# Kernel tuning notes

Measured on AMD Instinct MI355X. Metric: run time of the kernel, lower is better.

## Reference

```python
import jax, jax.numpy as jnp
import numpy as np

N, D, FIN, FOUT, H = 50000, 16, 256, 128, 128  # nodes, degree, in/out feat, lstm hidden


def setup_inputs() -> dict:
    key = jax.random.key(0)
    ks = jax.random.split(key, 16)
    E = N * D
    s = 1.0 / np.sqrt(H)
    inp = {
        "in_nodes_features": jax.random.normal(ks[0], (N, FIN), jnp.float32),
        "W_proj": jax.random.normal(ks[1], (FOUT, FIN), jnp.float32) * 0.05,
        "a_src": jax.random.normal(ks[2], (FOUT,), jnp.float32) * 0.1,
        "a_trg": jax.random.normal(ks[3], (FOUT,), jnp.float32) * 0.1,
        "W_skip": jax.random.normal(ks[4], (FOUT, FIN), jnp.float32) * 0.05,
        "bias": jnp.zeros((FOUT,), jnp.float32),
        "w_ih_f": jax.random.uniform(ks[5], (4 * H, FOUT), jnp.float32, -s, s),
        "w_hh_f": jax.random.uniform(ks[6], (4 * H, H), jnp.float32, -s, s),
        "b_ih_f": jax.random.uniform(ks[7], (4 * H,), jnp.float32, -s, s),
        "b_hh_f": jax.random.uniform(ks[8], (4 * H,), jnp.float32, -s, s),
        "w_ih_b": jax.random.uniform(ks[9], (4 * H, FOUT), jnp.float32, -s, s),
        "w_hh_b": jax.random.uniform(ks[10], (4 * H, H), jnp.float32, -s, s),
        "b_ih_b": jax.random.uniform(ks[11], (4 * H,), jnp.float32, -s, s),
        "b_hh_b": jax.random.uniform(ks[12], (4 * H,), jnp.float32, -s, s),
    }
    # uniform-degree graph: each node is target of exactly D edges (sorted by target)
    trg = jnp.repeat(jnp.arange(N, dtype=jnp.int32), D)
    src = jax.random.randint(ks[13], (E,), 0, N, dtype=jnp.int32)
    inp["edge_index"] = jnp.stack([src, trg])  # [2, E]
    return inp


def _lstm_final_h(seq, w_ih, w_hh, b_ih, b_hh):
    # seq: [N, T, F] -> final hidden state [N, H]
    h0 = jnp.zeros((seq.shape[0], w_hh.shape[1]), seq.dtype)
    def step(carry, x_t):
        h, c = carry
        gates = x_t @ w_ih.T + h @ w_hh.T + (b_ih + b_hh)
        i, f, g, o = jnp.split(gates, 4, axis=-1)
        c = jax.nn.sigmoid(f) * c + jax.nn.sigmoid(i) * jnp.tanh(g)
        h = jax.nn.sigmoid(o) * jnp.tanh(c)
        return (h, c), None
    (h, _), _ = jax.lax.scan(step, (h0, h0), jnp.swapaxes(seq, 0, 1))
    return h


def reference(in_nodes_features, W_proj, a_src, a_trg, W_skip, bias,
              w_ih_f, w_hh_f, b_ih_f, b_hh_f, w_ih_b, w_hh_b, b_ih_b, b_hh_b,
              edge_index):
    x = in_nodes_features
    n = x.shape[0]
    src, trg = edge_index[0], edge_index[1]
    proj = x @ W_proj.T                                   # [N, FOUT]
    s_src = proj @ a_src                                  # [N]
    s_trg = proj @ a_trg                                  # [N]
    # lift to edges
    scores = jax.nn.leaky_relu(s_src[src] + s_trg[trg], 0.2)   # [E]
    # neighborhood-aware softmax (global max subtraction as in original)
    e = jnp.exp(scores - jnp.max(scores))
    denom = jax.ops.segment_sum(e, trg, num_segments=n)
    att = e / (denom[trg] + 1e-16)                        # [E]
    weighted = proj[src] * att[:, None]                   # [E, FOUT]
    # trg is sorted with uniform degree: reshape to per-node neighbor sequences
    deg = weighted.shape[0] // n
    att_r = att.reshape(n, deg)
    feat_r = weighted.reshape(n, deg, -1)
    order = jnp.argsort(att_r, axis=1)                    # ascending attention, per node
    seq = jnp.take_along_axis(feat_r, order[:, :, None], axis=1)  # [N, D, FOUT]
    # bidirectional LSTM; hn[-1] == backward-direction final hidden
    out = _lstm_final_h(seq[:, ::-1], w_ih_b, w_hh_b, b_ih_b, b_hh_b)  # [N, H]
    # skip + bias + activation (dims differ -> skip_proj)
    out = out + x @ W_skip.T
    out = out + bias
    return jax.nn.leaky_relu(out, 0.01)
```

## Files before the change

### kernel.cpp

```cpp
#include <hip/hip_runtime.h>
#include <hip/hip_bf16.h>
#include <math.h>

#define N_NODES 50000
#define DEG 16
#define FIN 256
#define FOUT 128
#define HID 128
#define FG 512
#define NEDGE (N_NODES*DEG)
#define NCHUNK (N_NODES/16)
#define K5GRID 512

typedef __bf16 bf16x8 __attribute__((ext_vector_type(8)));
typedef float  f32x4  __attribute__((ext_vector_type(4)));

static __device__ __forceinline__ float u2f(unsigned int u){ union {unsigned int u; float f;} v; v.u=u; return v.f; }
static __device__ __forceinline__ unsigned int f2u(float f){ union {float f; unsigned int u;} v; v.f=f; return v.u; }
static __device__ __forceinline__ unsigned short f2bfu(float f){
  unsigned int u = f2u(f);
  unsigned int r = u + 0x7fffu + ((u >> 16) & 1u);
  return (unsigned short)(r >> 16);
}
static __device__ __forceinline__ float bflo(unsigned int u){ return u2f(u << 16); }
static __device__ __forceinline__ float bfhi(unsigned int u){ return u2f(u & 0xffff0000u); }
static __device__ __forceinline__ float rcpf(float x){ return __builtin_amdgcn_rcpf(x); }
static __device__ __forceinline__ float sigm(float x){ return rcpf(1.f + __expf(-x)); }
static __device__ __forceinline__ float tanhx(float x){ return 1.f - 2.f*rcpf(__expf(2.f*x) + 1.f); }

union FU { bf16x8 bf; unsigned short us[8]; uint4 u4; };

__global__ __launch_bounds__(256) void k_w(
    const float* __restrict__ Wp, const float* __restrict__ Ws,
    const float* __restrict__ wih, const float* __restrict__ a_src, const float* __restrict__ a_trg,
    unsigned short* __restrict__ Wch, unsigned short* __restrict__ Wcl,
    unsigned short* __restrict__ wihh, unsigned short* __restrict__ wihl,
    double* __restrict__ vsrc, double* __restrict__ vtrg,
    unsigned int* __restrict__ gmax_key)
{
  const int b = blockIdx.x, tid = threadIdx.x;
  if (b < 256) {
    const float* src = (b < 128) ? (Wp + b*FIN) : (Ws + (b-128)*FIN);
    const float v = src[tid];
    const unsigned short h = f2bfu(v);
    Wch[b*FIN + tid] = h;
    Wcl[b*FIN + tid] = f2bfu(v - u2f((unsigned)h << 16));
  } else if (b < 512) {
    const int row = (b-256)*2 + (tid >> 7);
    const int k   = tid & 127;
    const float v = wih[row*HID + k];
    const unsigned short h = f2bfu(v);
    wihh[row*HID + k] = h;
    wihl[row*HID + k] = f2bfu(v - u2f((unsigned)h << 16));
  } else {
    if (tid == 0) *gmax_key = 0u;
    const int k = tid;
    double s1 = 0.0, s2 = 0.0;
    for (int i = 0; i < FOUT; ++i) {
      const double w = (double)Wp[i*FIN + k];
      s1 += (double)a_src[i] * w;
      s2 += (double)a_trg[i] * w;
    }
    vsrc[k] = s1; vtrg[k] = s2;
  }
}

__global__ __launch_bounds__(256) void k_s(
    const float* __restrict__ x, const double* __restrict__ vsrc, const double* __restrict__ vtrg,
    double* __restrict__ ssrc, double* __restrict__ strg)
{
  const int n = blockIdx.x*256 + threadIdx.x;
  if (n >= N_NODES) return;
  double ss = 0.0, st = 0.0;
  for (int k = 0; k < FIN; k += 4) {
    const float4 xv = *(const float4*)&x[n*FIN + k];
    ss += xv.x*vsrc[k] + xv.y*vsrc[k+1] + xv.z*vsrc[k+2] + xv.w*vsrc[k+3];
    st += xv.x*vtrg[k] + xv.y*vtrg[k+1] + xv.z*vtrg[k+2] + xv.w*vtrg[k+3];
  }
  ssrc[n] = ss; strg[n] = st;
}

template<int KD, int MODE>
__global__ __launch_bounds__(256) void kgemm(
    const float* __restrict__ Af32,
    const unsigned short* __restrict__ Ah_g, const unsigned short* __restrict__ Al_g,
    const unsigned short* __restrict__ Bh_g, const unsigned short* __restrict__ Bl_g,
    const float* __restrict__ bias, float* __restrict__ outf,
    unsigned short* __restrict__ o_h, unsigned short* __restrict__ o_l)
{
  __shared__ unsigned short At[2][128*64];
  __shared__ unsigned short Bt[2][64*64];
  const int tid = threadIdx.x;
  const int bm = blockIdx.x, bn = blockIdx.y;
  const int r0 = bm*128;
  const int wave = tid >> 6, lane = tid & 63, c = lane & 15, q = lane >> 4;
  const int srow = tid >> 3, sg = tid & 7;

  f32x4 acc[2][4];
  #pragma unroll
  for (int rt = 0; rt < 2; ++rt)
    #pragma unroll
    for (int ct = 0; ct < 4; ++ct) acc[rt][ct] = (f32x4){0.f,0.f,0.f,0.f};

  for (int kt = 0; kt < KD/64; ++kt) {
    const int k0 = kt*64;
    __syncthreads();
    #pragma unroll
    for (int rr = 0; rr < 4; ++rr) {
      const int row = rr*32 + srow;
      int grow = r0 + row; if (grow >= N_NODES) grow = N_NODES-1;
      const int ga = grow*KD + k0 + sg*8;
      const int la = row*64 + (((sg ^ (row & 7))) << 3);
      if (MODE == 0) {
        const float4 v0 = *(const float4*)&Af32[ga];
        const float4 v1 = *(const float4*)&Af32[ga + 4];
        union { unsigned short us[8]; uint4 u4; } H, L;
        H.us[0]=f2bfu(v0.x); L.us[0]=f2bfu(v0.x - u2f((unsigned)H.us[0] << 16));
        H.us[1]=f2bfu(v0.y); L.us[1]=f2bfu(v0.y - u2f((unsigned)H.us[1] << 16));
        H.us[2]=f2bfu(v0.z); L.us[2]=f2bfu(v0.z - u2f((unsigned)H.us[2] << 16));
        H.us[3]=f2bfu(v0.w); L.us[3]=f2bfu(v0.w - u2f((unsigned)H.us[3] << 16));
        H.us[4]=f2bfu(v1.x); L.us[4]=f2bfu(v1.x - u2f((unsigned)H.us[4] << 16));
        H.us[5]=f2bfu(v1.y); L.us[5]=f2bfu(v1.y - u2f((unsigned)H.us[5] << 16));
        H.us[6]=f2bfu(v1.z); L.us[6]=f2bfu(v1.z - u2f((unsigned)H.us[6] << 16));
        H.us[7]=f2bfu(v1.w); L.us[7]=f2bfu(v1.w - u2f((unsigned)H.us[7] << 16));
        *(uint4*)&At[0][la] = H.u4;
        *(uint4*)&At[1][la] = L.u4;
      } else {
        *(uint4*)&At[0][la] = *(const uint4*)&Ah_g[ga];
        *(uint4*)&At[1][la] = *(const uint4*)&Al_g[ga];
      }
    }
    #pragma unroll
    for (int rr = 0; rr < 2; ++rr) {
      const int row = rr*32 + srow;
      int wr;
      if (MODE == 0) wr = bn*64 + row;
      else { const int j = bn*64 + row; wr = (j & 3)*HID + (j >> 2); }
      const int ga = wr*KD + k0 + sg*8;
      const int la = row*64 + (((sg ^ (row & 7))) << 3);
      *(uint4*)&Bt[0][la] = *(const uint4*)&Bh_g[ga];
      *(uint4*)&Bt[1][la] = *(const uint4*)&Bl_g[ga];
    }
    __syncthreads();

    #pragma unroll
    for (int s = 0; s < 2; ++s) {
      FU Af[2][2], Bf[4][2];
      #pragma unroll
      for (int rt = 0; rt < 2; ++rt) {
        const int row = wave*32 + rt*16 + c;
        const int ad = row*64 + (((((s<<2)+q) ^ (row & 7))) << 3);
        Af[rt][0].u4 = *(const uint4*)&At[0][ad];
        Af[rt][1].u4 = *(const uint4*)&At[1][ad];
      }
      #pragma unroll
      for (int ct = 0; ct < 4; ++ct) {
        const int row = ct*16 + c;
        const int ad = row*64 + (((((s<<2)+q) ^ (row & 7))) << 3);
        Bf[ct][0].u4 = *(const uint4*)&Bt[0][ad];
        Bf[ct][1].u4 = *(const uint4*)&Bt[1][ad];
      }
      #pragma unroll
      for (int rt = 0; rt < 2; ++rt)
        #pragma unroll
        for (int ct = 0; ct < 4; ++ct) {
          acc[rt][ct] = __builtin_amdgcn_mfma_f32_16x16x32_bf16(Af[rt][0].bf, Bf[ct][0].bf, acc[rt][ct], 0,0,0);
          acc[rt][ct] = __builtin_amdgcn_mfma_f32_16x16x32_bf16(Af[rt][1].bf, Bf[ct][0].bf, acc[rt][ct], 0,0,0);
          acc[rt][ct] = __builtin_amdgcn_mfma_f32_16x16x32_bf16(Af[rt][0].bf, Bf[ct][1].bf, acc[rt][ct], 0,0,0);
        }
    }
  }
  __syncthreads();

  if (MODE == 0 && bn >= 2) {
    #pragma unroll
    for (int ct = 0; ct < 4; ++ct) {
      const int col = bn*64 + ct*16 + c - 128;
      const float bv = bias[col];
      #pragma unroll
      for (int rt = 0; rt < 2; ++rt)
        #pragma unroll
        for (int i = 0; i < 4; ++i) {
          const int row = r0 + wave*32 + rt*16 + q*4 + i;
          if (row < N_NODES) outf[row*FOUT + col] = acc[rt][ct][i] + bv;
        }
    }
  } else {
    #pragma unroll
    for (int rt = 0; rt < 2; ++rt)
      #pragma unroll
      for (int ct = 0; ct < 4; ++ct)
        #pragma unroll
        for (int i = 0; i < 4; ++i) {
          const int lrow = wave*32 + rt*16 + q*4 + i;
          const int lcol = ct*16 + c;
          const float v = acc[rt][ct][i];
          const unsigned short h = f2bfu(v);
          At[0][lrow*64 + lcol] = h;
          if (MODE == 0) At[1][lrow*64 + lcol] = f2bfu(v - u2f((unsigned)h << 16));
        }
    __syncthreads();
    const int ncols = (MODE == 0) ? FOUT : FG;
    #pragma unroll
    for (int rr = 0; rr < 4; ++rr) {
      const int row = rr*32 + srow;
      const int grow = r0 + row;
      if (grow < N_NODES) {
        const int dst = grow*ncols + bn*64 + sg*8;
        *(uint4*)&o_h[dst] = *(const uint4*)&At[0][row*64 + sg*8];
        if (MODE == 0) *(uint4*)&o_l[dst] = *(const uint4*)&At[1][row*64 + sg*8];
      }
    }
  }
}

__global__ __launch_bounds__(256) void k3_scores(
    const double* __restrict__ ssrc, const double* __restrict__ strg,
    const int* __restrict__ esrc, const int* __restrict__ etrg,
    double* __restrict__ scod, unsigned int* __restrict__ gmax_key)
{
  const int n = blockIdx.x*256 + threadIdx.x;
  float lmax = -3.0e38f;
  if (n < N_NODES) {
    const double stn = strg[etrg[n*DEG]];
    #pragma unroll
    for (int j = 0; j < DEG; ++j) {
      const int e = n*DEG + j;
      double sc = ssrc[esrc[e]] + stn;
      sc = (sc > 0.0) ? sc : 0.2*sc;
      scod[e] = sc;
      lmax = fmaxf(lmax, (float)sc);
    }
  }
  #pragma unroll
  for (int off = 32; off > 0; off >>= 1)
    lmax = fmaxf(lmax, __shfl_down(lmax, off, 64));
  __shared__ float wmax[4];
  if ((threadIdx.x & 63) == 0) wmax[threadIdx.x >> 6] = lmax;
  __syncthreads();
  if (threadIdx.x == 0) {
    const float mv = fmaxf(fmaxf(wmax[0], wmax[1]), fmaxf(wmax[2], wmax[3]));
    const unsigned int u = f2u(mv);
    const unsigned int key = (u & 0x80000000u) ? ~u : (u | 0x80000000u);
    atomicMax(gmax_key, key);
  }
}

__global__ __launch_bounds__(256) void k4_att(
    const double* __restrict__ scod, const int* __restrict__ esrc,
    const unsigned int* __restrict__ gmax_key,
    float* __restrict__ atts, int* __restrict__ srcs)
{
  const int n = blockIdx.x*256 + threadIdx.x;
  if (n >= N_NODES) return;
  const unsigned int key = *gmax_key;
  const unsigned int u = (key & 0x80000000u) ? (key ^ 0x80000000u) : ~key;
  const float gmax = u2f(u);

  double sc[DEG]; float av[DEG]; int si[DEG];
  float sum = 0.f;
  #pragma unroll
  for (int j = 0; j < DEG; ++j) {
    sc[j] = scod[n*DEG + j];
    av[j] = __expf((float)sc[j] - gmax);
    sum  += av[j];
    si[j] = esrc[n*DEG + j];
  }
  const float inv = 1.f/(sum + 1e-16f);
  #pragma unroll
  for (int j = 0; j < DEG; ++j) {
    int r = 0;
    #pragma unroll
    for (int k = 0; k < DEG; ++k)
      r += (sc[k] > sc[j]) || (sc[k] == sc[j] && k > j);
    atts[n*DEG + r] = av[j]*inv;
    srcs[n*DEG + r] = si[j];
  }
}

__global__ __launch_bounds__(512, 4) void k5_lstm(
    const __hip_bfloat16* __restrict__ G, const float* __restrict__ whh,
    const float* __restrict__ bih, const float* __restrict__ bhh,
    const float* __restrict__ atts, const int* __restrict__ srcs,
    float* __restrict__ out)
{
  __shared__ unsigned short Bs[32768];
  __shared__ unsigned short hbuf[2][16*128];
  __shared__ float attb[16][16];
  __shared__ int   srcb[16][16];

  const int tid  = threadIdx.x;
  const int wave = tid >> 6;
  const int lane = tid & 63;
  const int c    = lane & 15;
  const int q    = lane >> 4;
  const int fcol = wave*16 + c;
  const int nb0  = q*4;

  #pragma unroll
  for (int j = 0; j < 8; ++j) {
    const int s   = tid + j*512;
    const int sg_ = s >> 11, skt = (s >> 9) & 3, sw8 = (s >> 6) & 7, sl = s & 63;
    const float* p = whh + (((sg_ + 2)*128 + sw8*16 + (sl & 15))*128 + skt*32 + (sl >> 4)*8);
    const float4 v0 = *(const float4*)p;
    const float4 v1 = *(const float4*)(p + 4);
    union { unsigned short us[8]; uint4 u4; } P;
    P.us[0]=f2bfu(v0.x); P.us[1]=f2bfu(v0.y); P.us[2]=f2bfu(v0.z); P.us[3]=f2bfu(v0.w);
    P.us[4]=f2bfu(v1.x); P.us[5]=f2bfu(v1.y); P.us[6]=f2bfu(v1.z); P.us[7]=f2bfu(v1.w);
    *(uint4*)&Bs[s*8] = P.u4;
  }

  FU Brg[2][4];
  #pragma unroll
  for (int g = 0; g < 2; ++g) {
    const float* wr = whh + (g*HID + fcol)*HID + q*8;
    #pragma unroll
    for (int kt = 0; kt < 4; ++kt) {
      const float4 w0 = *(const float4*)(wr + kt*32);
      const float4 w1 = *(const float4*)(wr + kt*32 + 4);
      Brg[g][kt].us[0]=f2bfu(w0.x); Brg[g][kt].us[1]=f2bfu(w0.y);
      Brg[g][kt].us[2]=f2bfu(w0.z); Brg[g][kt].us[3]=f2bfu(w0.w);
      Brg[g][kt].us[4]=f2bfu(w1.x); Brg[g][kt].us[5]=f2bfu(w1.y);
      Brg[g][kt].us[6]=f2bfu(w1.z); Brg[g][kt].us[7]=f2bfu(w1.w);
    }
  }

  float bsum[4];
  #pragma unroll
  for (int g = 0; g < 4; ++g) bsum[g] = bih[g*HID + fcol] + bhh[g*HID + fcol];

  int aoff[4];
  #pragma unroll
  for (int kt = 0; kt < 4; ++kt)
    aoff[kt] = c*128 + (((kt*4 + q) ^ c) & 15)*8;

  const unsigned short* Gu = (const unsigned short*)G;

  for (int chunk = blockIdx.x; chunk < NCHUNK; chunk += K5GRID) {
    const int nb = chunk * 16;
    __syncthreads();
    if (tid < 256) {
      ((float*)attb)[tid] = atts[nb*DEG + tid];
      ((int*)  srcb)[tid] = srcs[nb*DEG + tid];
    }
    __syncthreads();

    float cst[4] = {0.f,0.f,0.f,0.f};
    float hv[4]  = {0.f,0.f,0.f,0.f};
    uint2 pf[4];
    #pragma unroll
    for (int r = 0; r < 4; ++r) {
      const int s = srcb[nb0 + r][0];
      pf[r] = *(const uint2*)(Gu + (size_t)s*FG + fcol*4);
    }

    #pragma unroll 4
    for (int t = 0; t < DEG; ++t) {
      uint2 cur[4]; float at[4];
      #pragma unroll
      for (int r = 0; r < 4; ++r) { cur[r] = pf[r]; at[r] = attb[nb0 + r][t]; }
      if (t < DEG-1) {
        #pragma unroll
        for (int r = 0; r < 4; ++r) {
          const int s = srcb[nb0 + r][t+1];
          pf[r] = *(const uint2*)(Gu + (size_t)s*FG + fcol*4);
        }
      }
      f32x4 acc[4];
      #pragma unroll
      for (int r = 0; r < 4; ++r) {
        acc[0][r] = bsum[0] + at[r]*bflo(cur[r].x);
        acc[1][r] = bsum[1] + at[r]*bfhi(cur[r].x);
        acc[2][r] = bsum[2] + at[r]*bflo(cur[r].y);
        acc[3][r] = bsum[3] + at[r]*bfhi(cur[r].y);
      }
      if (t > 0) {
        __syncthreads();
        const unsigned short* hb = hbuf[(t-1) & 1];
        FU A[4];
        #pragma unroll
        for (int kt = 0; kt < 4; ++kt) A[kt].u4 = *(const uint4*)(hb + aoff[kt]);
        #pragma unroll
        for (int g = 0; g < 2; ++g) {
          #pragma unroll
          for (int kt = 0; kt < 4; ++kt)
            acc[g] = __builtin_amdgcn_mfma_f32_16x16x32_bf16(A[kt].bf, Brg[g][kt].bf, acc[g], 0, 0, 0);
        }
        #pragma unroll
        for (int g = 2; g < 4; ++g) {
          FU Bf[4];
          #pragma unroll
          for (int kt = 0; kt < 4; ++kt)
            Bf[kt].u4 = *(const uint4*)&Bs[((((g-2)*4 + kt)*8 + wave)*64 + lane)*8];
          #pragma unroll
          for (int kt = 0; kt < 4; ++kt)
            acc[g] = __builtin_amdgcn_mfma_f32_16x16x32_bf16(A[kt].bf, Bf[kt].bf, acc[g], 0, 0, 0);
        }
      }
      #pragma unroll
      for (int r = 0; r < 4; ++r) {
        const float ig = sigm (acc[0][r]);
        const float fg = sigm (acc[1][r]);
        const float gg = tanhx(acc[2][r]);
        const float og = sigm (acc[3][r]);
        cst[r] = fg*cst[r] + ig*gg;
        hv[r]  = og*tanhx(cst[r]);
      }
      if (t < DEG-1) {
        unsigned short* hw = hbuf[t & 1];
        #pragma unroll
        for (int r = 0; r < 4; ++r) {
          const float other = __shfl_xor(hv[r], 1, 64);
          if ((c & 1) == 0) {
            const unsigned pack = (unsigned)f2bfu(hv[r]) | ((unsigned)f2bfu(other) << 16);
            const int node = nb0 + r;
            const int k = fcol;
            const int half = node*128 + (((k >> 3) ^ node) & 15)*8 + (k & 7);
            *(unsigned*)(hw + half) = pack;
          }
        }
      }
    }
    #pragma unroll
    for (int r = 0; r < 4; ++r) {
      const int node = nb + nb0 + r;
      const float v = hv[r] + out[node*HID + fcol];
      out[node*HID + fcol] = (v > 0.f) ? v : 0.01f*v;
    }
  }
}

extern "C" void kernel_launch(void* const* d_in, const int* in_sizes, int n_in,
                              void* d_out, int out_size, void* d_ws, size_t ws_size,
                              hipStream_t stream)
{
  (void)in_sizes; (void)n_in; (void)out_size; (void)ws_size;
  const float* x     = (const float*)d_in[0];
  const float* Wp    = (const float*)d_in[1];
  const float* a_src = (const float*)d_in[2];
  const float* a_trg = (const float*)d_in[3];
  const float* Ws    = (const float*)d_in[4];
  const float* bias  = (const float*)d_in[5];
  const float* wih_b = (const float*)d_in[10];
  const float* whh_b = (const float*)d_in[11];
  const float* bih_b = (const float*)d_in[12];
  const float* bhh_b = (const float*)d_in[13];
  const int*   eidx  = (const int*)d_in[14];
  const int* esrc = eidx;
  const int* etrg = eidx + NEDGE;
  float* out = (float*)d_out;

  unsigned char* ws = (unsigned char*)d_ws;
  unsigned int*   gmax = (unsigned int*)(ws + 0);
  unsigned short* Gh   = (unsigned short*)(ws + 256);
  unsigned short* projh= (unsigned short*)(ws + 51200256);
  unsigned short* projl= (unsigned short*)(ws + 64000256);
  double*         scod = (double*)(ws + 51200256);
  float*          atts = (float*) (ws + 64000256);
  int*            srcs = (int*)   (ws + 67200256);
  unsigned short* Wch  = (unsigned short*)(ws + 76800256);
  unsigned short* Wcl  = (unsigned short*)(ws + 76931328);
  unsigned short* wihh = (unsigned short*)(ws + 77062400);
  unsigned short* wihl = (unsigned short*)(ws + 77193472);
  double*         vsrc = (double*)(ws + 77324544);
  double*         vtrg = (double*)(ws + 77326592);
  double*         ssrc = (double*)(ws + 77328640);
  double*         strg = (double*)(ws + 77728640);

  k_w<<<dim3(513), dim3(256), 0, stream>>>(Wp, Ws, wih_b, a_src, a_trg,
                                           Wch, Wcl, wihh, wihl, vsrc, vtrg, gmax);
  k_s<<<dim3((N_NODES+255)/256), dim3(256), 0, stream>>>(x, vsrc, vtrg, ssrc, strg);
  kgemm<FIN,0><<<dim3((N_NODES+127)/128, 4), dim3(256), 0, stream>>>(
      x, (const unsigned short*)0, (const unsigned short*)0, Wch, Wcl, bias, out, projh, projl);
  kgemm<HID,1><<<dim3((N_NODES+127)/128, 8), dim3(256), 0, stream>>>(
      (const float*)0, projh, projl, wihh, wihl, bias, out, Gh, (unsigned short*)0);
  k3_scores<<<dim3((N_NODES+255)/256), dim3(256), 0, stream>>>(ssrc, strg, esrc, etrg, scod, gmax);
  k4_att<<<dim3((N_NODES+255)/256), dim3(256), 0, stream>>>(scod, esrc, gmax, atts, srcs);
  k5_lstm<<<dim3(K5GRID), dim3(512), 0, stream>>>((const __hip_bfloat16*)Gh, whh_b, bih_b, bhh_b, atts, srcs, out);
}
```

Before: 505.6 us.

## Fuse score and attention kernels using per-node max, parallelize score dot products

Merges the edge-score kernel and the softmax/sort kernel into one, replacing the global-max atomic with a per-node max. Per-node max subtraction is mathematically equivalent for the softmax, and it removes a kernel launch, the double-precision score buffer round trip, and the atomic. The node-score kernel now uses one wave per node with a shuffle reduction instead of one thread per node doing a serial 256-element loop, which gives coalesced loads. Source indices are pre-multiplied by the row stride so the LSTM gather skips a multiply. Underflow behaviour can differ slightly from the global-max reference.

```diff
diff --git a/kernel.cpp b/kernel.cpp
--- a/kernel.cpp
+++ b/kernel.cpp
@@ -35,8 +35,7 @@
     const float* __restrict__ wih, const float* __restrict__ a_src, const float* __restrict__ a_trg,
     unsigned short* __restrict__ Wch, unsigned short* __restrict__ Wcl,
     unsigned short* __restrict__ wihh, unsigned short* __restrict__ wihl,
-    double* __restrict__ vsrc, double* __restrict__ vtrg,
-    unsigned int* __restrict__ gmax_key)
+    double* __restrict__ vsrc, double* __restrict__ vtrg)
 {
   const int b = blockIdx.x, tid = threadIdx.x;
   if (b < 256) {
@@ -53,7 +52,6 @@
     wihh[row*HID + k] = h;
     wihl[row*HID + k] = f2bfu(v - u2f((unsigned)h << 16));
   } else {
-    if (tid == 0) *gmax_key = 0u;
     const int k = tid;
     double s1 = 0.0, s2 = 0.0;
     for (int i = 0; i < FOUT; ++i) {
@@ -69,15 +67,19 @@
     const float* __restrict__ x, const double* __restrict__ vsrc, const double* __restrict__ vtrg,
     double* __restrict__ ssrc, double* __restrict__ strg)
 {
-  const int n = blockIdx.x*256 + threadIdx.x;
+  const int wave = threadIdx.x >> 6, lane = threadIdx.x & 63;
+  const int n = blockIdx.x*4 + wave;
   if (n >= N_NODES) return;
-  double ss = 0.0, st = 0.0;
-  for (int k = 0; k < FIN; k += 4) {
-    const float4 xv = *(const float4*)&x[n*FIN + k];
-    ss += xv.x*vsrc[k] + xv.y*vsrc[k+1] + xv.z*vsrc[k+2] + xv.w*vsrc[k+3];
-    st += xv.x*vtrg[k] + xv.y*vtrg[k+1] + xv.z*vtrg[k+2] + xv.w*vtrg[k+3];
-  }
-  ssrc[n] = ss; strg[n] = st;
+  const float4 xv = *(const float4*)&x[n*FIN + lane*4];
+  const double x0 = xv.x, x1 = xv.y, x2 = xv.z, x3 = xv.w;
+  double a = x0*vsrc[lane*4] + x1*vsrc[lane*4+1] + x2*vsrc[lane*4+2] + x3*vsrc[lane*4+3];
+  double b = x0*vtrg[lane*4] + x1*vtrg[lane*4+1] + x2*vtrg[lane*4+2] + x3*vtrg[lane*4+3];
+  #pragma unroll
+  for (int off = 32; off > 0; off >>= 1) {
+    a += __shfl_down(a, off, 64);
+    b += __shfl_down(b, off, 64);
+  }
+  if (lane == 0) { ssrc[n] = a; strg[n] = b; }
 }
 
 template<int KD, int MODE>
@@ -214,57 +216,31 @@
   }
 }
 
-__global__ __launch_bounds__(256) void k3_scores(
+__global__ __launch_bounds__(256) void k34(
     const double* __restrict__ ssrc, const double* __restrict__ strg,
     const int* __restrict__ esrc, const int* __restrict__ etrg,
-    double* __restrict__ scod, unsigned int* __restrict__ gmax_key)
-{
-  const int n = blockIdx.x*256 + threadIdx.x;
-  float lmax = -3.0e38f;
-  if (n < N_NODES) {
-    const double stn = strg[etrg[n*DEG]];
-    #pragma unroll
-    for (int j = 0; j < DEG; ++j) {
-      const int e = n*DEG + j;
-      double sc = ssrc[esrc[e]] + stn;
-      sc = (sc > 0.0) ? sc : 0.2*sc;
-      scod[e] = sc;
-      lmax = fmaxf(lmax, (float)sc);
-    }
-  }
-  #pragma unroll
-  for (int off = 32; off > 0; off >>= 1)
-    lmax = fmaxf(lmax, __shfl_down(lmax, off, 64));
-  __shared__ float wmax[4];
-  if ((threadIdx.x & 63) == 0) wmax[threadIdx.x >> 6] = lmax;
-  __syncthreads();
-  if (threadIdx.x == 0) {
-    const float mv = fmaxf(fmaxf(wmax[0], wmax[1]), fmaxf(wmax[2], wmax[3]));
-    const unsigned int u = f2u(mv);
-    const unsigned int key = (u & 0x80000000u) ? ~u : (u | 0x80000000u);
-    atomicMax(gmax_key, key);
-  }
-}
-
-__global__ __launch_bounds__(256) void k4_att(
-    const double* __restrict__ scod, const int* __restrict__ esrc,
-    const unsigned int* __restrict__ gmax_key,
     float* __restrict__ atts, int* __restrict__ srcs)
 {
   const int n = blockIdx.x*256 + threadIdx.x;
   if (n >= N_NODES) return;
-  const unsigned int key = *gmax_key;
-  const unsigned int u = (key & 0x80000000u) ? (key ^ 0x80000000u) : ~key;
-  const float gmax = u2f(u);
-
-  double sc[DEG]; float av[DEG]; int si[DEG];
-  float sum = 0.f;
+  const double stn = strg[etrg[n*DEG]];
+  double sc[DEG]; int si[DEG];
+  double mx = -1.0e300;
   #pragma unroll
   for (int j = 0; j < DEG; ++j) {
-    sc[j] = scod[n*DEG + j];
-    av[j] = __expf((float)sc[j] - gmax);
-    sum  += av[j];
-    si[j] = esrc[n*DEG + j];
+    const int s = esrc[n*DEG + j];
+    double v = ssrc[s] + stn;
+    v = (v > 0.0) ? v : 0.2*v;
+    sc[j] = v;
+    mx = (v > mx) ? v : mx;
+    si[j] = s;
+  }
+  const float mxf = (float)mx;
+  float av[DEG]; float sum = 0.f;
+  #pragma unroll
+  for (int j = 0; j < DEG; ++j) {
+    av[j] = __expf((float)sc[j] - mxf);
+    sum += av[j];
   }
   const float inv = 1.f/(sum + 1e-16f);
   #pragma unroll
@@ -274,7 +250,7 @@
     for (int k = 0; k < DEG; ++k)
       r += (sc[k] > sc[j]) || (sc[k] == sc[j] && k > j);
     atts[n*DEG + r] = av[j]*inv;
-    srcs[n*DEG + r] = si[j];
+    srcs[n*DEG + r] = si[j]*FG;
   }
 }
 
@@ -350,8 +326,8 @@
     uint2 pf[4];
     #pragma unroll
     for (int r = 0; r < 4; ++r) {
-      const int s = srcb[nb0 + r][0];
-      pf[r] = *(const uint2*)(Gu + (size_t)s*FG + fcol*4);
+      const int so = srcb[nb0 + r][0];
+      pf[r] = *(const uint2*)(Gu + (size_t)so + fcol*4);
     }
 
     #pragma unroll 4
@@ -362,8 +338,8 @@
       if (t < DEG-1) {
         #pragma unroll
         for (int r = 0; r < 4; ++r) {
-          const int s = srcb[nb0 + r][t+1];
-          pf[r] = *(const uint2*)(Gu + (size_t)s*FG + fcol*4);
+          const int so = srcb[nb0 + r][t+1];
+          pf[r] = *(const uint2*)(Gu + (size_t)so + fcol*4);
         }
       }
       f32x4 acc[4];
@@ -451,11 +427,9 @@
   float* out = (float*)d_out;
 
   unsigned char* ws = (unsigned char*)d_ws;
-  unsigned int*   gmax = (unsigned int*)(ws + 0);
   unsigned short* Gh   = (unsigned short*)(ws + 256);
   unsigned short* projh= (unsigned short*)(ws + 51200256);
   unsigned short* projl= (unsigned short*)(ws + 64000256);
-  double*         scod = (double*)(ws + 51200256);
   float*          atts = (float*) (ws + 64000256);
   int*            srcs = (int*)   (ws + 67200256);
   unsigned short* Wch  = (unsigned short*)(ws + 76800256);
@@ -468,13 +442,12 @@
   double*         strg = (double*)(ws + 77728640);
 
   k_w<<<dim3(513), dim3(256), 0, stream>>>(Wp, Ws, wih_b, a_src, a_trg,
-                                           Wch, Wcl, wihh, wihl, vsrc, vtrg, gmax);
-  k_s<<<dim3((N_NODES+255)/256), dim3(256), 0, stream>>>(x, vsrc, vtrg, ssrc, strg);
+                                           Wch, Wcl, wihh, wihl, vsrc, vtrg);
+  k_s<<<dim3((N_NODES+3)/4), dim3(256), 0, stream>>>(x, vsrc, vtrg, ssrc, strg);
   kgemm<FIN,0><<<dim3((N_NODES+127)/128, 4), dim3(256), 0, stream>>>(
       x, (const unsigned short*)0, (const unsigned short*)0, Wch, Wcl, bias, out, projh, projl);
   kgemm<HID,1><<<dim3((N_NODES+127)/128, 8), dim3(256), 0, stream>>>(
       (const float*)0, projh, projl, wihh, wihl, bias, out, Gh, (unsigned short*)0);
-  k3_scores<<<dim3((N_NODES+255)/256), dim3(256), 0, stream>>>(ssrc, strg, esrc, etrg, scod, gmax);
-  k4_att<<<dim3((N_NODES+255)/256), dim3(256), 0, stream>>>(scod, esrc, gmax, atts, srcs);
+  k34<<<dim3((N_NODES+255)/256), dim3(256), 0, stream>>>(ssrc, strg, esrc, etrg, atts, srcs);
   k5_lstm<<<dim3(K5GRID), dim3(512), 0, stream>>>((const __hip_bfloat16*)Gh, whh_b, bih_b, bhh_b, atts, srcs, out);
 }
```

Result: faster. 459.3 us (-9.2%).
